# Optimization experiments

Hardware: AMD Instinct MI355X
Metric: run time of the kernel (lower is better)

Reference implementation:

```python
import jax, jax.numpy as jnp
import numpy as np


def setup_inputs() -> dict:
    key = jax.random.key(0)
    k1, k2, k3 = jax.random.split(key, 3)
    x = jax.random.normal(k1, (16, 128, 128, 64), dtype=jnp.float32)
    kernel = jax.random.normal(k2, (3, 3, 64, 128), dtype=jnp.float32) * 0.05
    bias = jax.random.normal(k3, (128,), dtype=jnp.float32) * 0.05
    return {"x": x, "kernel": kernel, "bias": bias}


def reference(x, kernel, bias):
    # Faithful to myconv2d: extract_patches (stride 1, rate 1, SAME) followed by
    # per-out-channel multiply+reduce over the flattened (kh*kw*cin) patch axis,
    # which is mathematically a stride-1 SAME conv2d. Expressed as a direct conv.
    out = jax.lax.conv_general_dilated(
        x, kernel,
        window_strides=(1, 1),
        padding="SAME",
        dimension_numbers=("NHWC", "HWIO", "NHWC"),
    )
    return out + bias  # bias broadcast over channel dim, as in call()
```

## Files before the change

### kernel.cpp

```cpp
#include <hip/hip_runtime.h>


#define HH 128
#define WW 128
#define CIN 64
#define COUT 128

typedef __attribute__((ext_vector_type(8))) short v8s;
typedef __attribute__((ext_vector_type(4))) float v4f;

#define ROW_CHUNKS 1040
#define WS_NEEDED  (9u * CIN * COUT * 2u)

static __device__ __forceinline__ unsigned short f2bf(float f) {
    unsigned int u = __float_as_uint(f);
    unsigned int r = (u + 0x7fffu + ((u >> 16) & 1u)) >> 16;
    return (unsigned short)r;
}

__global__ __launch_bounds__(256) void cvt_w(const float* __restrict__ wgt,
                                             unsigned short* __restrict__ wt) {
    int idx = blockIdx.x * 256 + threadIdx.x;
    if (idx >= 9 * CIN * COUT) return;
    int co  = idx & (COUT - 1);
    int ci  = (idx >> 7) & (CIN - 1);
    int tap = idx >> 13;
    int kc  = ci >> 5;
    int cl  = ci & 31;
    wt[((tap * 2 + kc) * COUT + co) * 32 + cl] = f2bf(wgt[idx]);
}

__global__ __launch_bounds__(256, 3) void conv_mfma(
    const float* __restrict__ x,
    const unsigned short* __restrict__ wt,
    const float* __restrict__ bias,
    float* __restrict__ out) {
    __shared__ v8s smem[3 * ROW_CHUNKS];

    int bid = blockIdx.x;
    int logical = ((bid & 7) << 8) | (bid >> 3);
    int h = logical & (HH - 1);
    int n = logical >> 7;

    int tid  = threadIdx.x;
    int lane = tid & 63;
    int wid  = tid >> 6;
    int l15  = lane & 15;
    int quad = lane >> 4;

    if (tid < 48) {
        int row = tid >> 4, k = tid & 15;
        int c = (k < 8) ? k : (1024 + k);
        smem[row * ROW_CHUNKS + c] = (v8s)(short)0;
    }

    #pragma unroll
    for (int dh = 0; dh < 3; ++dh) {
        int ih = h + dh - 1;
        v8s* dst = smem + dh * ROW_CHUNKS;
        if (ih >= 0 && ih < HH) {
            const float* rowf = x + ((size_t)(n * HH + ih)) * WW * CIN;
            #pragma unroll
            for (int k = 0; k < 4; ++k) {
                int c = 8 + tid + (k << 8);
                const float* p = rowf + (size_t)(c - 8) * 8;
                float4 a = *(const float4*)p;
                float4 b = *(const float4*)(p + 4);
                v8s ch;
                ch[0] = (short)f2bf(a.x); ch[1] = (short)f2bf(a.y);
                ch[2] = (short)f2bf(a.z); ch[3] = (short)f2bf(a.w);
                ch[4] = (short)f2bf(b.x); ch[5] = (short)f2bf(b.y);
                ch[6] = (short)f2bf(b.z); ch[7] = (short)f2bf(b.w);
                dst[c ^ ((c >> 3) & 7)] = ch;
            }
        } else {
            #pragma unroll
            for (int k = 0; k < 4; ++k) {
                int c = 8 + tid + (k << 8);
                dst[c ^ ((c >> 3) & 7)] = (v8s)(short)0;
            }
        }
    }

    const unsigned short* wlane = wt + ((size_t)(wid * 32 + l15)) * 32 + quad * 8;

    v8s bb[3][2];
    #pragma unroll
    for (int tj = 0; tj < 2; ++tj) {
        bb[0][tj] = *(const v8s*)(wlane + 0 * 4096 + tj * 512);
        bb[1][tj] = *(const v8s*)(wlane + 1 * 4096 + tj * 512);
    }

    __syncthreads();

    v4f acc[8][2];
    #pragma unroll
    for (int i = 0; i < 8; ++i)
        #pragma unroll
        for (int j = 0; j < 2; ++j) acc[i][j] = (v4f)0.f;

    #pragma unroll
    for (int s = 0; s < 18; ++s) {
        const int tap = s >> 1;
        const int dh  = tap / 3;
        const int dw  = tap % 3;
        const int kc  = s & 1;
        const int cur = s % 3;

        if (s < 16) {
            const int nb = (s + 2) % 3;
            #pragma unroll
            for (int tj = 0; tj < 2; ++tj)
                bb[nb][tj] = *(const v8s*)(wlane + (s + 2) * 4096 + tj * 512);
        }

        const v8s* srow = smem + dh * ROW_CHUNKS;
        const int pl0 = l15 + dw;
        const int sw  = pl0 & 7;
        const int c0  = pl0 * 8 + kc * 4 + quad;

        v8s a0 = srow[(c0 + 0 * 128) ^ sw];
        v8s a1 = srow[(c0 + 1 * 128) ^ sw];
        #pragma unroll
        for (int tj = 0; tj < 2; ++tj)
            acc[0][tj] = __builtin_amdgcn_mfma_f32_16x16x32_bf16(
                a0, bb[cur][tj], acc[0][tj], 0, 0, 0);
        v8s a2 = srow[(c0 + 2 * 128) ^ sw];
        #pragma unroll
        for (int tj = 0; tj < 2; ++tj)
            acc[1][tj] = __builtin_amdgcn_mfma_f32_16x16x32_bf16(
                a1, bb[cur][tj], acc[1][tj], 0, 0, 0);
        v8s a3 = srow[(c0 + 3 * 128) ^ sw];
        #pragma unroll
        for (int tj = 0; tj < 2; ++tj)
            acc[2][tj] = __builtin_amdgcn_mfma_f32_16x16x32_bf16(
                a2, bb[cur][tj], acc[2][tj], 0, 0, 0);
        v8s a4 = srow[(c0 + 4 * 128) ^ sw];
        #pragma unroll
        for (int tj = 0; tj < 2; ++tj)
            acc[3][tj] = __builtin_amdgcn_mfma_f32_16x16x32_bf16(
                a3, bb[cur][tj], acc[3][tj], 0, 0, 0);
        v8s a5 = srow[(c0 + 5 * 128) ^ sw];
        #pragma unroll
        for (int tj = 0; tj < 2; ++tj)
            acc[4][tj] = __builtin_amdgcn_mfma_f32_16x16x32_bf16(
                a4, bb[cur][tj], acc[4][tj], 0, 0, 0);
        v8s a6 = srow[(c0 + 6 * 128) ^ sw];
        #pragma unroll
        for (int tj = 0; tj < 2; ++tj)
            acc[5][tj] = __builtin_amdgcn_mfma_f32_16x16x32_bf16(
                a5, bb[cur][tj], acc[5][tj], 0, 0, 0);
        v8s a7 = srow[(c0 + 7 * 128) ^ sw];
        #pragma unroll
        for (int tj = 0; tj < 2; ++tj)
            acc[6][tj] = __builtin_amdgcn_mfma_f32_16x16x32_bf16(
                a6, bb[cur][tj], acc[6][tj], 0, 0, 0);
        #pragma unroll
        for (int tj = 0; tj < 2; ++tj)
            acc[7][tj] = __builtin_amdgcn_mfma_f32_16x16x32_bf16(
                a7, bb[cur][tj], acc[7][tj], 0, 0, 0);
    }

    float bv[2];
    #pragma unroll
    for (int tj = 0; tj < 2; ++tj) bv[tj] = bias[wid * 32 + tj * 16 + l15];

    float* orow = out + ((size_t)(n * HH + h)) * WW * COUT;
    #pragma unroll
    for (int ti = 0; ti < 8; ++ti) {
        #pragma unroll
        for (int r = 0; r < 4; ++r) {
            int p = ti * 16 + quad * 4 + r;
            float* op = orow + (size_t)p * COUT + wid * 32 + l15;
            op[0]  = acc[ti][0][r] + bv[0];
            op[16] = acc[ti][1][r] + bv[1];
        }
    }
}

__global__ __launch_bounds__(256) void conv3x3_direct(
    const float* __restrict__ x, const float* __restrict__ wgt,
    const float* __restrict__ bias, float* __restrict__ out) {
    int idx = blockIdx.x * 256 + threadIdx.x;
    int co = idx & (COUT - 1);
    int w  = (idx >> 7) & (WW - 1);
    int h  = (idx >> 14) & (HH - 1);
    int n  = idx >> 21;
    float acc = bias[co];
    #pragma unroll
    for (int kh = 0; kh < 3; ++kh) {
        int ih = h + kh - 1;
        if (ih < 0 || ih >= HH) continue;
        #pragma unroll
        for (int kw = 0; kw < 3; ++kw) {
            int iw = w + kw - 1;
            if (iw < 0 || iw >= WW) continue;
            const float* xp = x + (((size_t)(n * HH + ih) * WW + iw) * CIN);
            const float* wp = wgt + ((size_t)((kh * 3 + kw) * CIN)) * COUT + co;
            #pragma unroll 8
            for (int ci = 0; ci < CIN; ++ci)
                acc = fmaf(xp[ci], wp[(size_t)ci * COUT], acc);
        }
    }
    out[idx] = acc;
}

extern "C" void kernel_launch(void* const* d_in, const int* in_sizes, int n_in,
                              void* d_out, int out_size, void* d_ws, size_t ws_size,
                              hipStream_t stream) {
    const float* x    = (const float*)d_in[0];
    const float* wgt  = (const float*)d_in[1];
    const float* bias = (const float*)d_in[2];
    float* out = (float*)d_out;

    if (ws_size < (size_t)WS_NEEDED) {
        int blocks = (out_size + 255) / 256;
        conv3x3_direct<<<blocks, 256, 0, stream>>>(x, wgt, bias, out);
        return;
    }

    unsigned short* wt = (unsigned short*)d_ws;
    cvt_w<<<(9 * CIN * COUT + 255) / 256, 256, 0, stream>>>(wgt, wt);
    conv_mfma<<<16 * HH, 256, 0, stream>>>(x, wt, bias, out);
}
```

Measured before the change: 212.3 us.

## Split each output row into two 64-pixel halves per block

Each block now computes half an output row (64 pixels) instead of a full row, which doubles the grid to 4096 blocks. Shared memory per block shrinks to 3 halo rows of 66 pixels, and accumulators drop from 8x2 to 4x2 tiles. The goal is more parallelism and occupancy from lower LDS and register use. In exchange, the weight loads and halo input are re-read per half-row, so there is more redundant global traffic and less MFMA work per B-fragment load.

```diff
diff --git a/kernel.cpp b/kernel.cpp
--- a/kernel.cpp
+++ b/kernel.cpp
@@ -9,7 +9,7 @@
 typedef __attribute__((ext_vector_type(8))) short v8s;
 typedef __attribute__((ext_vector_type(4))) float v4f;
 
-#define ROW_CHUNKS 1040
+#define ROW_CHUNKS 528
 #define WS_NEEDED  (9u * CIN * COUT * 2u)
 
 static __device__ __forceinline__ unsigned short f2bf(float f) {
@@ -38,9 +38,11 @@
     __shared__ v8s smem[3 * ROW_CHUNKS];
 
     int bid = blockIdx.x;
-    int logical = ((bid & 7) << 8) | (bid >> 3);
-    int h = logical & (HH - 1);
-    int n = logical >> 7;
+    int logical = ((bid & 7) << 9) | (bid >> 3);
+    int wh = logical & 1;
+    int h  = (logical >> 1) & (HH - 1);
+    int n  = logical >> 8;
+    int w0 = wh << 6;
 
     int tid  = threadIdx.x;
     int lane = tid & 63;
@@ -48,42 +50,34 @@
     int l15  = lane & 15;
     int quad = lane >> 4;
 
-    if (tid < 48) {
-        int row = tid >> 4, k = tid & 15;
-        int c = (k < 8) ? k : (1024 + k);
-        smem[row * ROW_CHUNKS + c] = (v8s)(short)0;
-    }
-
     #pragma unroll
     for (int dh = 0; dh < 3; ++dh) {
         int ih = h + dh - 1;
+        bool rowok = (ih >= 0) && (ih < HH);
+        const float* rowf = x + ((size_t)(n * HH + (rowok ? ih : 0))) * WW * CIN;
         v8s* dst = smem + dh * ROW_CHUNKS;
-        if (ih >= 0 && ih < HH) {
-            const float* rowf = x + ((size_t)(n * HH + ih)) * WW * CIN;
-            #pragma unroll
-            for (int k = 0; k < 4; ++k) {
-                int c = 8 + tid + (k << 8);
-                const float* p = rowf + (size_t)(c - 8) * 8;
-                float4 a = *(const float4*)p;
-                float4 b = *(const float4*)(p + 4);
-                v8s ch;
-                ch[0] = (short)f2bf(a.x); ch[1] = (short)f2bf(a.y);
-                ch[2] = (short)f2bf(a.z); ch[3] = (short)f2bf(a.w);
-                ch[4] = (short)f2bf(b.x); ch[5] = (short)f2bf(b.y);
-                ch[6] = (short)f2bf(b.z); ch[7] = (short)f2bf(b.w);
-                dst[c ^ ((c >> 3) & 7)] = ch;
+        #pragma unroll
+        for (int k = 0; k < 3; ++k) {
+            int c = tid + (k << 8);
+            if (c < ROW_CHUNKS) {
+                int lp = c >> 3;
+                int gp = w0 - 1 + lp;
+                v8s ch = (v8s)(short)0;
+                if (rowok && gp >= 0 && gp < WW) {
+                    const float* p = rowf + gp * CIN + (c & 7) * 8;
+                    float4 a = *(const float4*)p;
+                    float4 b = *(const float4*)(p + 4);
+                    ch[0] = (short)f2bf(a.x); ch[1] = (short)f2bf(a.y);
+                    ch[2] = (short)f2bf(a.z); ch[3] = (short)f2bf(a.w);
+                    ch[4] = (short)f2bf(b.x); ch[5] = (short)f2bf(b.y);
+                    ch[6] = (short)f2bf(b.z); ch[7] = (short)f2bf(b.w);
+                }
+                dst[c ^ (lp & 7)] = ch;
             }
-        } else {
-            #pragma unroll
-            for (int k = 0; k < 4; ++k) {
-                int c = 8 + tid + (k << 8);
-                dst[c ^ ((c >> 3) & 7)] = (v8s)(short)0;
-            }
         }
     }
 
     const unsigned short* wlane = wt + ((size_t)(wid * 32 + l15)) * 32 + quad * 8;
-
     v8s bb[3][2];
     #pragma unroll
     for (int tj = 0; tj < 2; ++tj) {
@@ -93,9 +87,9 @@
 
     __syncthreads();
 
-    v4f acc[8][2];
-    #pragma unroll
-    for (int i = 0; i < 8; ++i)
+    v4f acc[4][2];
+    #pragma unroll
+    for (int i = 0; i < 4; ++i)
         #pragma unroll
         for (int j = 0; j < 2; ++j) acc[i][j] = (v4f)0.f;
 
@@ -115,9 +109,9 @@
         }
 
         const v8s* srow = smem + dh * ROW_CHUNKS;
-        const int pl0 = l15 + dw;
-        const int sw  = pl0 & 7;
-        const int c0  = pl0 * 8 + kc * 4 + quad;
+        const int lp0 = l15 + dw;
+        const int sw  = lp0 & 7;
+        const int c0  = lp0 * 8 + kc * 4 + quad;
 
         v8s a0 = srow[(c0 + 0 * 128) ^ sw];
         v8s a1 = srow[(c0 + 1 * 128) ^ sw];
@@ -135,43 +129,24 @@
         for (int tj = 0; tj < 2; ++tj)
             acc[2][tj] = __builtin_amdgcn_mfma_f32_16x16x32_bf16(
                 a2, bb[cur][tj], acc[2][tj], 0, 0, 0);
-        v8s a4 = srow[(c0 + 4 * 128) ^ sw];
         #pragma unroll
         for (int tj = 0; tj < 2; ++tj)
             acc[3][tj] = __builtin_amdgcn_mfma_f32_16x16x32_bf16(
                 a3, bb[cur][tj], acc[3][tj], 0, 0, 0);
-        v8s a5 = srow[(c0 + 5 * 128) ^ sw];
-        #pragma unroll
-        for (int tj = 0; tj < 2; ++tj)
-            acc[4][tj] = __builtin_amdgcn_mfma_f32_16x16x32_bf16(
-                a4, bb[cur][tj], acc[4][tj], 0, 0, 0);
-        v8s a6 = srow[(c0 + 6 * 128) ^ sw];
-        #pragma unroll
-        for (int tj = 0; tj < 2; ++tj)
-            acc[5][tj] = __builtin_amdgcn_mfma_f32_16x16x32_bf16(
-                a5, bb[cur][tj], acc[5][tj], 0, 0, 0);
-        v8s a7 = srow[(c0 + 7 * 128) ^ sw];
-        #pragma unroll
-        for (int tj = 0; tj < 2; ++tj)
-            acc[6][tj] = __builtin_amdgcn_mfma_f32_16x16x32_bf16(
-                a6, bb[cur][tj], acc[6][tj], 0, 0, 0);
-        #pragma unroll
-        for (int tj = 0; tj < 2; ++tj)
-            acc[7][tj] = __builtin_amdgcn_mfma_f32_16x16x32_bf16(
-                a7, bb[cur][tj], acc[7][tj], 0, 0, 0);
     }
 
     float bv[2];
     #pragma unroll
     for (int tj = 0; tj < 2; ++tj) bv[tj] = bias[wid * 32 + tj * 16 + l15];
 
-    float* orow = out + ((size_t)(n * HH + h)) * WW * COUT;
-    #pragma unroll
-    for (int ti = 0; ti < 8; ++ti) {
+    const float* __restrict__ ob =
+        out + ((size_t)(n * HH + h) * WW + w0) * COUT + wid * 32 + l15;
+    #pragma unroll
+    for (int ti = 0; ti < 4; ++ti) {
         #pragma unroll
         for (int r = 0; r < 4; ++r) {
             int p = ti * 16 + quad * 4 + r;
-            float* op = orow + (size_t)p * COUT + wid * 32 + l15;
+            float* op = (float*)ob + (size_t)p * COUT;
             op[0]  = acc[ti][0][r] + bv[0];
             op[16] = acc[ti][1][r] + bv[1];
         }
@@ -221,5 +196,5 @@
 
     unsigned short* wt = (unsigned short*)d_ws;
     cvt_w<<<(9 * CIN * COUT + 255) / 256, 256, 0, stream>>>(wgt, wt);
-    conv_mfma<<<16 * HH, 256, 0, stream>>>(x, wt, bias, out);
-}
+    conv_mfma<<<16 * HH * 2, 256, 0, stream>>>(x, wt, bias, out);
+}
```

New measurement: 228.9 us. 7.8% more time.
